# Performance work log

Measured on AMD Instinct MI355X. Metric: run time of the kernel, lower is better.

## Reference

```python
import jax, jax.numpy as jnp
import numpy as np

B, T, E = 4, 2048, 768
H = 12
D = E // H  # head dim = 64


def setup_inputs() -> dict:
    key = jax.random.key(0)
    ks = jax.random.split(key, 9)
    s = 0.02
    x = jax.random.normal(ks[0], (B, T, E), dtype=jnp.float32)
    Wq = jax.random.normal(ks[1], (E, E), dtype=jnp.float32) * s
    bq = jnp.zeros((E,), dtype=jnp.float32)
    Wk = jax.random.normal(ks[2], (E, E), dtype=jnp.float32) * s
    bk = jnp.zeros((E,), dtype=jnp.float32)
    Wv = jax.random.normal(ks[3], (E, E), dtype=jnp.float32) * s
    bv = jnp.zeros((E,), dtype=jnp.float32)
    Wo = jax.random.normal(ks[4], (E, E), dtype=jnp.float32) * s
    bo = jnp.zeros((E,), dtype=jnp.float32)
    # causal mask, broadcastable [1,1,T,T]; masked_fill where mask == 0
    attn_mask = jnp.tril(jnp.ones((T, T), dtype=jnp.int32))[None, None, :, :]
    return {"x": x, "Wq": Wq, "bq": bq, "Wk": Wk, "bk": bk,
            "Wv": Wv, "bv": bv, "Wo": Wo, "bo": bo, "attn_mask": attn_mask}


def reference(x, Wq, bq, Wk, bk, Wv, bv, Wo, bo, attn_mask):
    # QKV projections: [B,T,E] -> [B,T,E]
    q = x @ Wq + bq
    k = x @ Wk + bk
    v = x @ Wv + bv
    # split heads -> [B,H,T,D]
    def split(t):
        return t.reshape(B, T, H, D).transpose(0, 2, 1, 3)
    q, k, v = split(q), split(k), split(v)
    # eager attention: full [B,H,T,T] scores (faithful to the torch module)
    att = jnp.einsum('bhqd,bhkd->bhqk', q, k) * (1.0 / np.sqrt(D).astype(np.float32))
    att = jnp.where(attn_mask == 0, jnp.float32(-jnp.inf), att)
    att_weights = jax.nn.softmax(att, axis=-1)
    # attn_dropout rate = 0.0 (eval) -> identity
    y = jnp.einsum('bhqk,bhkd->bhqd', att_weights, v)
    y = y.transpose(0, 2, 1, 3).reshape(B, T, E)
    y = y @ Wo + bo  # proj_dropout rate = 0.0 -> identity
    return (y, att_weights)
```

## Files before the change

### kernel.cpp

```cpp
#include <hip/hip_runtime.h>
#include <hip/hip_bf16.h>
#include <stdint.h>

#define BB 4
#define HH 12
#define TT 2048
#define DD 64
#define EE 768
#define BT (BB*TT)
#define NQKV (3*EE)

typedef __attribute__((ext_vector_type(8))) short bf16x8;
typedef __attribute__((ext_vector_type(4))) float f32x4;

__device__ __forceinline__ unsigned short f2bf(float f){
  union { float f; unsigned int u; } x; x.f = f;
  unsigned int u = x.u;
  unsigned int r = (u + 0x7fffu + ((u >> 16) & 1u)) >> 16;
  return (unsigned short)r;
}

__global__ void cvt_bf16(const float* __restrict__ src, unsigned short* __restrict__ dst, int n){
  int i = (blockIdx.x*blockDim.x + threadIdx.x)*4;
  if (i < n){
    float4 v = *(const float4*)&src[i];
    ushort4 o;
    o.x = f2bf(v.x); o.y = f2bf(v.y); o.z = f2bf(v.z); o.w = f2bf(v.w);
    *(ushort4*)&dst[i] = o;
  }
}

__global__ void transpose_cvt_768(const float* __restrict__ src,
                                  unsigned short* __restrict__ dst){
  __shared__ float tile[32][33];
  int bx = blockIdx.x*32, by = blockIdx.y*32;
  int tx = threadIdx.x, ty = threadIdx.y;
  #pragma unroll
  for (int i=0;i<32;i+=8) tile[ty+i][tx] = src[(size_t)(by+ty+i)*EE + bx+tx];
  __syncthreads();
  #pragma unroll
  for (int i=0;i<32;i+=8) dst[(size_t)(bx+ty+i)*EE + by+tx] = f2bf(tile[tx][ty+i]);
}

__device__ __forceinline__ void gemm_core_128(
    const unsigned short* __restrict__ A, const unsigned short* __restrict__ Bt,
    int K, int mBase, int nBase,
    unsigned short* Alds, unsigned short* Blds,
    f32x4 acc[4][4])
{
  const int tid = threadIdx.x;
  const int lane = tid & 63, wave = tid >> 6;
  const int wm = wave & 1, wn = wave >> 1;
  const int ln15 = lane & 15, quad = lane >> 4;
  #pragma unroll
  for (int mt=0; mt<4; ++mt)
    #pragma unroll
    for (int nt=0; nt<4; ++nt)
      acc[mt][nt] = (f32x4){0.f,0.f,0.f,0.f};

  for (int k0=0; k0<K; k0+=32){
    #pragma unroll
    for (int i=0;i<2;i++){
      int idx = tid + i*256;
      int r = idx >> 2, seg = idx & 3;
      *(uint4*)&Alds[r*40 + seg*8] = *(const uint4*)&A[(size_t)(mBase + r)*K + k0 + seg*8];
      *(uint4*)&Blds[r*40 + seg*8] = *(const uint4*)&Bt[(size_t)(nBase + r)*K + k0 + seg*8];
    }
    __syncthreads();
    bf16x8 af[4], bfr[4];
    #pragma unroll
    for (int mt=0;mt<4;++mt) af[mt]  = *(const bf16x8*)&Alds[(wm*64 + mt*16 + ln15)*40 + quad*8];
    #pragma unroll
    for (int nt=0;nt<4;++nt) bfr[nt] = *(const bf16x8*)&Blds[(wn*64 + nt*16 + ln15)*40 + quad*8];
    #pragma unroll
    for (int mt=0;mt<4;++mt)
      #pragma unroll
      for (int nt=0;nt<4;++nt)
        acc[mt][nt] = __builtin_amdgcn_mfma_f32_16x16x32_bf16(af[mt], bfr[nt], acc[mt][nt], 0,0,0);
    __syncthreads();
  }
}

#define QSCALE 0.18033688f
__global__ __launch_bounds__(256,2) void gemm_qkv(
    const unsigned short* __restrict__ x, const unsigned short* __restrict__ WtQKV,
    const float* __restrict__ bq, const float* __restrict__ bk,
    const float* __restrict__ bv,
    unsigned short* __restrict__ q_ws, unsigned short* __restrict__ k_ws,
    unsigned short* __restrict__ v_ws)
{
  __shared__ unsigned short Alds[128*40];
  __shared__ unsigned short Blds[128*40];
  const int mBase = blockIdx.y*128, nBase = blockIdx.x*128;
  f32x4 acc[4][4];
  gemm_core_128(x, WtQKV, EE, mBase, nBase, Alds, Blds, acc);

  const int tid = threadIdx.x, lane = tid&63, wave = tid>>6;
  const int wm = wave&1, wn = wave>>1, ln15 = lane&15, quad = lane>>4;
  const int which = nBase / EE;
  const float* bias = (which==0) ? bq : ((which==1) ? bk : bv);
  const float sc = (which==0) ? QSCALE : 1.0f;
  #pragma unroll
  for (int nt=0;nt<4;++nt){
    int col = nBase + wn*64 + nt*16 + ln15;
    int n0 = col - which*EE;
    int h = n0 >> 6, d = n0 & 63;
    float bsv = bias[n0];
    #pragma unroll
    for (int mt=0;mt<4;++mt){
      #pragma unroll
      for (int reg=0;reg<4;++reg){
        int row = mBase + wm*64 + mt*16 + quad*4 + reg;
        int b = row >> 11, t = row & 2047;
        unsigned short o = f2bf((acc[mt][nt][reg] + bsv)*sc);
        if (which==0)      q_ws[((size_t)(b*HH + h)*TT + t)*DD + d] = o;
        else if (which==1) k_ws[((size_t)(b*HH + h)*TT + t)*DD + d] = o;
        else               v_ws[((size_t)(b*HH + h)*DD + d)*TT + t] = o;
      }
    }
  }
}

__global__ __launch_bounds__(256,2) void gemm_proj(
    const unsigned short* __restrict__ yin, const unsigned short* __restrict__ WoT,
    const float* __restrict__ bo, float* __restrict__ out)
{
  __shared__ unsigned short Alds[128*40];
  __shared__ unsigned short Blds[128*40];
  const int mBase = blockIdx.y*128, nBase = blockIdx.x*128;
  f32x4 acc[4][4];
  gemm_core_128(yin, WoT, EE, mBase, nBase, Alds, Blds, acc);

  const int tid = threadIdx.x, lane = tid&63, wave = tid>>6;
  const int wm = wave&1, wn = wave>>1, ln15 = lane&15, quad = lane>>4;
  #pragma unroll
  for (int nt=0;nt<4;++nt){
    int col = nBase + wn*64 + nt*16 + ln15;
    float bsv = bo[col];
    #pragma unroll
    for (int mt=0;mt<4;++mt){
      #pragma unroll
      for (int reg=0;reg<4;++reg){
        int row = mBase + wm*64 + mt*16 + quad*4 + reg;
        out[(size_t)row*EE + col] = acc[mt][nt][reg] + bsv;
      }
    }
  }
}

__global__ __launch_bounds__(256,2) void attn_kernel(
    const unsigned short* __restrict__ q_ws, const unsigned short* __restrict__ k_ws,
    const unsigned short* __restrict__ v_ws, float* __restrict__ att,
    unsigned short* __restrict__ y_ws)
{
  const int sid = blockIdx.x;
  const int qt  = (sid >> 3) & 31;
  const int bh  = (sid & 7) + ((sid >> 8) << 3);
  const int b  = bh / HH, h = bh - b*HH;
  const int tid = threadIdx.x, lane = tid&63, wave = tid>>6;
  const int quad = lane>>4, ln15 = lane&15;

  __shared__ unsigned short Qs[64*72];
  __shared__ unsigned short Ks[2][64*72];
  __shared__ unsigned short Vts[2][64*72];
  __shared__ unsigned short Ps[4*16*72];

  const unsigned short* Qg = q_ws + ((size_t)bh*TT + qt*64)*DD;
  const unsigned short* Kg = k_ws + (size_t)bh*TT*DD;
  const unsigned short* Vg = v_ws + (size_t)bh*DD*TT;
  float* attb = att + ((size_t)bh*TT + (size_t)qt*64)*TT;

  const int r0 = tid>>3, sg = tid&7;
  const int r1 = r0 + 32;

  uint4 ka0 = *(const uint4*)&Kg[(size_t)r0*DD + sg*8];
  uint4 ka1 = *(const uint4*)&Kg[(size_t)r1*DD + sg*8];

  *(uint4*)&Qs[r0*72 + sg*8] = *(const uint4*)&Qg[(size_t)r0*DD + sg*8];
  *(uint4*)&Qs[r1*72 + sg*8] = *(const uint4*)&Qg[(size_t)r1*DD + sg*8];
  __syncthreads();
  bf16x8 aq0 = *(const bf16x8*)&Qs[(wave*16+ln15)*72 + quad*8];
  bf16x8 aq1 = *(const bf16x8*)&Qs[(wave*16+ln15)*72 + 32 + quad*8];

  const float NEG = -30000.0f;
  const int qrow0 = qt*64 + wave*16 + quad*4;

  float lp[4] = {0.f,0.f,0.f,0.f};
  for (int kt=0; kt<=qt; ++kt){
    unsigned short* Kb = Ks[kt&1];
    *(uint4*)&Kb[r0*72 + sg*8] = ka0;
    *(uint4*)&Kb[r1*72 + sg*8] = ka1;
    __syncthreads();
    if (kt < qt){
      ka0 = *(const uint4*)&Kg[(size_t)((kt+1)*64+r0)*DD + sg*8];
      ka1 = *(const uint4*)&Kg[(size_t)((kt+1)*64+r1)*DD + sg*8];
    }
    f32x4 s[4];
    #pragma unroll
    for (int nt=0;nt<4;++nt){
      s[nt] = (f32x4){0.f,0.f,0.f,0.f};
      bf16x8 bk0 = *(const bf16x8*)&Kb[(nt*16+ln15)*72 + quad*8];
      bf16x8 bk1 = *(const bf16x8*)&Kb[(nt*16+ln15)*72 + 32 + quad*8];
      s[nt] = __builtin_amdgcn_mfma_f32_16x16x32_bf16(aq0, bk0, s[nt], 0,0,0);
      s[nt] = __builtin_amdgcn_mfma_f32_16x16x32_bf16(aq1, bk1, s[nt], 0,0,0);
    }
    const bool diag = (kt==qt);
    #pragma unroll
    for (int reg=0;reg<4;++reg){
      #pragma unroll
      for (int nt=0;nt<4;++nt){
        float v = s[nt][reg];
        if (diag && (kt*64 + nt*16 + ln15) > qrow0+reg) v = NEG;
        lp[reg] += exp2f(v);
      }
    }
  }
  float rl[4];
  #pragma unroll
  for (int r=0;r<4;++r){
    float ss = lp[r];
    ss += __shfl_xor(ss, 1);
    ss += __shfl_xor(ss, 2);
    ss += __shfl_xor(ss, 4);
    ss += __shfl_xor(ss, 8);
    rl[r] = 1.f / ss;
  }

  f32x4 yacc[4];
  #pragma unroll
  for (int nt=0;nt<4;++nt) yacc[nt] = (f32x4){0.f,0.f,0.f,0.f};

  uint4 kb0 = *(const uint4*)&Kg[(size_t)r0*DD + sg*8];
  uint4 kb1 = *(const uint4*)&Kg[(size_t)r1*DD + sg*8];
  uint4 vb0 = *(const uint4*)&Vg[(size_t)r0*TT + sg*8];
  uint4 vb1 = *(const uint4*)&Vg[(size_t)r1*TT + sg*8];
  __syncthreads();

  for (int kt=0; kt<=qt; ++kt){
    unsigned short* Kb = Ks[kt&1];
    unsigned short* Vb = Vts[kt&1];
    *(uint4*)&Kb[r0*72 + sg*8] = kb0;
    *(uint4*)&Kb[r1*72 + sg*8] = kb1;
    *(uint4*)&Vb[r0*72 + sg*8] = vb0;
    *(uint4*)&Vb[r1*72 + sg*8] = vb1;
    __syncthreads();
    if (kt < qt){
      kb0 = *(const uint4*)&Kg[(size_t)((kt+1)*64+r0)*DD + sg*8];
      kb1 = *(const uint4*)&Kg[(size_t)((kt+1)*64+r1)*DD + sg*8];
      vb0 = *(const uint4*)&Vg[(size_t)r0*TT + (kt+1)*64 + sg*8];
      vb1 = *(const uint4*)&Vg[(size_t)r1*TT + (kt+1)*64 + sg*8];
    }
    f32x4 s[4];
    #pragma unroll
    for (int nt=0;nt<4;++nt){
      s[nt] = (f32x4){0.f,0.f,0.f,0.f};
      bf16x8 bk0 = *(const bf16x8*)&Kb[(nt*16+ln15)*72 + quad*8];
      bf16x8 bk1 = *(const bf16x8*)&Kb[(nt*16+ln15)*72 + 32 + quad*8];
      s[nt] = __builtin_amdgcn_mfma_f32_16x16x32_bf16(aq0, bk0, s[nt], 0,0,0);
      s[nt] = __builtin_amdgcn_mfma_f32_16x16x32_bf16(aq1, bk1, s[nt], 0,0,0);
    }
    const bool diag = (kt==qt);
    #pragma unroll
    for (int nt=0;nt<4;++nt){
      int key = kt*64 + nt*16 + ln15;
      #pragma unroll
      for (int reg=0;reg<4;++reg){
        float v = s[nt][reg];
        if (diag && key > qrow0+reg) v = NEG;
        float p = exp2f(v)*rl[reg];
        attb[(size_t)(wave*16 + quad*4 + reg)*TT + key] = p;
        Ps[wave*1152 + (quad*4+reg)*72 + nt*16 + ln15] = f2bf(p);
      }
    }
    bf16x8 ap0 = *(const bf16x8*)&Ps[(wave*16+ln15)*72 + quad*8];
    bf16x8 ap1 = *(const bf16x8*)&Ps[(wave*16+ln15)*72 + 32 + quad*8];
    #pragma unroll
    for (int nt=0;nt<4;++nt){
      bf16x8 bv0 = *(const bf16x8*)&Vb[(nt*16+ln15)*72 + quad*8];
      bf16x8 bv1 = *(const bf16x8*)&Vb[(nt*16+ln15)*72 + 32 + quad*8];
      yacc[nt] = __builtin_amdgcn_mfma_f32_16x16x32_bf16(ap0, bv0, yacc[nt], 0,0,0);
      yacc[nt] = __builtin_amdgcn_mfma_f32_16x16x32_bf16(ap1, bv1, yacc[nt], 0,0,0);
    }
  }

  {
    int wstart = (qt+1)*64;
    int r = tid>>2;
    float4 z = make_float4(0.f,0.f,0.f,0.f);
    for (int c = wstart + (tid&3)*4; c < TT; c += 16)
      *(float4*)&attb[(size_t)r*TT + c] = z;
  }

  #pragma unroll
  for (int nt=0;nt<4;++nt){
    #pragma unroll
    for (int reg=0;reg<4;++reg){
      int t = qt*64 + wave*16 + quad*4 + reg;
      size_t row = (size_t)b*TT + t;
      int col = h*DD + nt*16 + ln15;
      y_ws[row*EE + col] = f2bf(yacc[nt][reg]);
    }
  }
}

extern "C" void kernel_launch(void* const* d_in, const int* in_sizes, int n_in,
                              void* d_out, int out_size, void* d_ws, size_t ws_size,
                              hipStream_t stream){
  (void)in_sizes; (void)n_in; (void)out_size; (void)ws_size;
  const float* x  = (const float*)d_in[0];
  const float* Wq = (const float*)d_in[1];
  const float* bq = (const float*)d_in[2];
  const float* Wk = (const float*)d_in[3];
  const float* bk = (const float*)d_in[4];
  const float* Wv = (const float*)d_in[5];
  const float* bv = (const float*)d_in[6];
  const float* Wo = (const float*)d_in[7];
  const float* bo = (const float*)d_in[8];

  float* out = (float*)d_out;
  float* y_out   = out;
  float* att_out = out + (size_t)BT*EE;

  unsigned short* ws = (unsigned short*)d_ws;
  unsigned short* x_bf   = ws;
  unsigned short* WtQKV  = x_bf  + (size_t)BT*EE;
  unsigned short* WoT    = WtQKV + (size_t)NQKV*EE;
  unsigned short* q_ws   = WoT   + (size_t)EE*EE;
  unsigned short* k_ws   = q_ws  + (size_t)BB*HH*TT*DD;
  unsigned short* v_ws   = k_ws  + (size_t)BB*HH*TT*DD;
  unsigned short* y_ws   = v_ws  + (size_t)BB*HH*TT*DD;

  cvt_bf16<<<(BT*EE)/(256*4), 256, 0, stream>>>(x, x_bf, BT*EE);
  dim3 tb(32,8), tg(24,24);
  transpose_cvt_768<<<tg, tb, 0, stream>>>(Wq, WtQKV);
  transpose_cvt_768<<<tg, tb, 0, stream>>>(Wk, WtQKV + (size_t)EE*EE);
  transpose_cvt_768<<<tg, tb, 0, stream>>>(Wv, WtQKV + (size_t)2*EE*EE);
  transpose_cvt_768<<<tg, tb, 0, stream>>>(Wo, WoT);

  gemm_qkv<<<dim3(NQKV/128, BT/128), 256, 0, stream>>>(x_bf, WtQKV, bq, bk, bv, q_ws, k_ws, v_ws);
  attn_kernel<<<dim3(32*BB*HH), 256, 0, stream>>>(q_ws, k_ws, v_ws, att_out, y_ws);
  gemm_proj<<<dim3(EE/128, BT/128), 256, 0, stream>>>(y_ws, WoT, bo, y_out);
}
```

Before: 1.115 ms.

## Process two query tiles per attention block to share K/V tile loads

Each attention workgroup now handles 128 query rows (two 64-row subtiles) instead of 64, so each K and V tile staged into shared memory is reused by both subtiles, roughly halving K/V global traffic and LDS staging. The grid is halved and query tiles are scheduled in descending order so the longest causal blocks start first. The cost is more registers for the doubled accumulators and Q fragments, which may reduce occupancy, and fewer, larger blocks that can leave CUs idle at the tail.

```diff
diff --git a/kernel.cpp b/kernel.cpp
--- a/kernel.cpp
+++ b/kernel.cpp
@@ -153,152 +153,186 @@
     const unsigned short* __restrict__ v_ws, float* __restrict__ att,
     unsigned short* __restrict__ y_ws)
 {
-  const int sid = blockIdx.x;
-  const int qt  = (sid >> 3) & 31;
-  const int bh  = (sid & 7) + ((sid >> 8) << 3);
-  const int b  = bh / HH, h = bh - b*HH;
-  const int tid = threadIdx.x, lane = tid&63, wave = tid>>6;
-  const int quad = lane>>4, ln15 = lane&15;
-
-  __shared__ unsigned short Qs[64*72];
+  const int bid  = blockIdx.x;
+  const int grp  = bid >> 7;
+  const int qt   = 15 - ((bid >> 3) & 15);
+  const int bh   = (bid & 7) | (grp << 3);
+  const int b    = bh / HH;
+  const int h    = bh - b*HH;
+  const int tid  = threadIdx.x;
+  const int lane = tid & 63, wave = tid >> 6;
+  const int quad = lane >> 4, ln15 = lane & 15;
+  const int q0   = 2*qt;
+  const int q1   = q0 + 1;
+  const int qbase = qt*128;
+
+  __shared__ unsigned short Qs[128*72];
   __shared__ unsigned short Ks[2][64*72];
   __shared__ unsigned short Vts[2][64*72];
   __shared__ unsigned short Ps[4*16*72];
 
-  const unsigned short* Qg = q_ws + ((size_t)bh*TT + qt*64)*DD;
+  const unsigned short* Qg = q_ws + ((size_t)bh*TT + qbase)*DD;
   const unsigned short* Kg = k_ws + (size_t)bh*TT*DD;
   const unsigned short* Vg = v_ws + (size_t)bh*DD*TT;
-  float* attb = att + ((size_t)bh*TT + (size_t)qt*64)*TT;
-
-  const int r0 = tid>>3, sg = tid&7;
-  const int r1 = r0 + 32;
-
-  uint4 ka0 = *(const uint4*)&Kg[(size_t)r0*DD + sg*8];
-  uint4 ka1 = *(const uint4*)&Kg[(size_t)r1*DD + sg*8];
-
-  *(uint4*)&Qs[r0*72 + sg*8] = *(const uint4*)&Qg[(size_t)r0*DD + sg*8];
-  *(uint4*)&Qs[r1*72 + sg*8] = *(const uint4*)&Qg[(size_t)r1*DD + sg*8];
+  float* attb = att + ((size_t)bh*TT + (size_t)qbase)*TT;
+
+  const int seg  = tid & 7;
+  const int rowA = tid >> 3;
+  const int rowB = rowA + 32;
+
+  uint4 pkA = *(const uint4*)&Kg[(size_t)rowA*DD + seg*8];
+  uint4 pkB = *(const uint4*)&Kg[(size_t)rowB*DD + seg*8];
+
+  #pragma unroll
+  for (int i=0;i<4;i++){
+    int r = rowA + i*32;
+    *(uint4*)&Qs[r*72 + seg*8] = *(const uint4*)&Qg[(size_t)r*DD + seg*8];
+  }
   __syncthreads();
-  bf16x8 aq0 = *(const bf16x8*)&Qs[(wave*16+ln15)*72 + quad*8];
-  bf16x8 aq1 = *(const bf16x8*)&Qs[(wave*16+ln15)*72 + 32 + quad*8];
+  bf16x8 aq[2][2];
+  #pragma unroll
+  for (int st=0; st<2; ++st){
+    aq[st][0] = *(const bf16x8*)&Qs[(st*64 + wave*16+ln15)*72 + quad*8];
+    aq[st][1] = *(const bf16x8*)&Qs[(st*64 + wave*16+ln15)*72 + 32 + quad*8];
+  }
 
   const float NEG = -30000.0f;
-  const int qrow0 = qt*64 + wave*16 + quad*4;
-
-  float lp[4] = {0.f,0.f,0.f,0.f};
-  for (int kt=0; kt<=qt; ++kt){
+
+  float lp[2][4] = {{0.f,0.f,0.f,0.f},{0.f,0.f,0.f,0.f}};
+  for (int kt=0; kt<=q1; ++kt){
     unsigned short* Kb = Ks[kt&1];
-    *(uint4*)&Kb[r0*72 + sg*8] = ka0;
-    *(uint4*)&Kb[r1*72 + sg*8] = ka1;
+    *(uint4*)&Kb[rowA*72 + seg*8] = pkA;
+    *(uint4*)&Kb[rowB*72 + seg*8] = pkB;
     __syncthreads();
-    if (kt < qt){
-      ka0 = *(const uint4*)&Kg[(size_t)((kt+1)*64+r0)*DD + sg*8];
-      ka1 = *(const uint4*)&Kg[(size_t)((kt+1)*64+r1)*DD + sg*8];
-    }
-    f32x4 s[4];
-    #pragma unroll
-    for (int nt=0;nt<4;++nt){
-      s[nt] = (f32x4){0.f,0.f,0.f,0.f};
-      bf16x8 bk0 = *(const bf16x8*)&Kb[(nt*16+ln15)*72 + quad*8];
-      bf16x8 bk1 = *(const bf16x8*)&Kb[(nt*16+ln15)*72 + 32 + quad*8];
-      s[nt] = __builtin_amdgcn_mfma_f32_16x16x32_bf16(aq0, bk0, s[nt], 0,0,0);
-      s[nt] = __builtin_amdgcn_mfma_f32_16x16x32_bf16(aq1, bk1, s[nt], 0,0,0);
-    }
-    const bool diag = (kt==qt);
-    #pragma unroll
-    for (int reg=0;reg<4;++reg){
-      #pragma unroll
-      for (int nt=0;nt<4;++nt){
-        float v = s[nt][reg];
-        if (diag && (kt*64 + nt*16 + ln15) > qrow0+reg) v = NEG;
-        lp[reg] += exp2f(v);
-      }
-    }
-  }
-  float rl[4];
-  #pragma unroll
-  for (int r=0;r<4;++r){
-    float ss = lp[r];
-    ss += __shfl_xor(ss, 1);
-    ss += __shfl_xor(ss, 2);
-    ss += __shfl_xor(ss, 4);
-    ss += __shfl_xor(ss, 8);
-    rl[r] = 1.f / ss;
-  }
-
-  f32x4 yacc[4];
-  #pragma unroll
-  for (int nt=0;nt<4;++nt) yacc[nt] = (f32x4){0.f,0.f,0.f,0.f};
-
-  uint4 kb0 = *(const uint4*)&Kg[(size_t)r0*DD + sg*8];
-  uint4 kb1 = *(const uint4*)&Kg[(size_t)r1*DD + sg*8];
-  uint4 vb0 = *(const uint4*)&Vg[(size_t)r0*TT + sg*8];
-  uint4 vb1 = *(const uint4*)&Vg[(size_t)r1*TT + sg*8];
+    if (kt < q1){
+      pkA = *(const uint4*)&Kg[(size_t)((kt+1)*64+rowA)*DD + seg*8];
+      pkB = *(const uint4*)&Kg[(size_t)((kt+1)*64+rowB)*DD + seg*8];
+    }
+    #pragma unroll
+    for (int st=0; st<2; ++st){
+      if (kt <= q0 + st){
+        f32x4 s[4];
+        #pragma unroll
+        for (int nt=0;nt<4;++nt){
+          s[nt] = (f32x4){0.f,0.f,0.f,0.f};
+          bf16x8 bk0 = *(const bf16x8*)&Kb[(nt*16+ln15)*72 + quad*8];
+          bf16x8 bk1 = *(const bf16x8*)&Kb[(nt*16+ln15)*72 + 32 + quad*8];
+          s[nt] = __builtin_amdgcn_mfma_f32_16x16x32_bf16(aq[st][0], bk0, s[nt], 0,0,0);
+          s[nt] = __builtin_amdgcn_mfma_f32_16x16x32_bf16(aq[st][1], bk1, s[nt], 0,0,0);
+        }
+        const bool diag = (kt == q0 + st);
+        const int qr0 = qbase + st*64 + wave*16 + quad*4;
+        #pragma unroll
+        for (int reg=0;reg<4;++reg){
+          #pragma unroll
+          for (int nt=0;nt<4;++nt){
+            float v = s[nt][reg];
+            if (diag && (kt*64 + nt*16 + ln15) > qr0+reg) v = NEG;
+            lp[st][reg] += exp2f(v);
+          }
+        }
+      }
+    }
+  }
+  float rl[2][4];
+  #pragma unroll
+  for (int st=0; st<2; ++st){
+    #pragma unroll
+    for (int r=0;r<4;++r){
+      float ss = lp[st][r];
+      ss += __shfl_xor(ss, 1);
+      ss += __shfl_xor(ss, 2);
+      ss += __shfl_xor(ss, 4);
+      ss += __shfl_xor(ss, 8);
+      rl[st][r] = 1.f / ss;
+    }
+  }
+
+  f32x4 yacc[2][4];
+  #pragma unroll
+  for (int st=0; st<2; ++st)
+    #pragma unroll
+    for (int nt=0;nt<4;++nt) yacc[st][nt] = (f32x4){0.f,0.f,0.f,0.f};
+
+  uint4 pk2A = *(const uint4*)&Kg[(size_t)rowA*DD + seg*8];
+  uint4 pk2B = *(const uint4*)&Kg[(size_t)rowB*DD + seg*8];
+  uint4 pvA  = *(const uint4*)&Vg[(size_t)rowA*TT + seg*8];
+  uint4 pvB  = *(const uint4*)&Vg[(size_t)rowB*TT + seg*8];
   __syncthreads();
 
-  for (int kt=0; kt<=qt; ++kt){
+  for (int kt=0; kt<=q1; ++kt){
     unsigned short* Kb = Ks[kt&1];
     unsigned short* Vb = Vts[kt&1];
-    *(uint4*)&Kb[r0*72 + sg*8] = kb0;
-    *(uint4*)&Kb[r1*72 + sg*8] = kb1;
-    *(uint4*)&Vb[r0*72 + sg*8] = vb0;
-    *(uint4*)&Vb[r1*72 + sg*8] = vb1;
+    *(uint4*)&Kb[rowA*72 + seg*8] = pk2A;
+    *(uint4*)&Kb[rowB*72 + seg*8] = pk2B;
+    *(uint4*)&Vb[rowA*72 + seg*8] = pvA;
+    *(uint4*)&Vb[rowB*72 + seg*8] = pvB;
     __syncthreads();
-    if (kt < qt){
-      kb0 = *(const uint4*)&Kg[(size_t)((kt+1)*64+r0)*DD + sg*8];
-      kb1 = *(const uint4*)&Kg[(size_t)((kt+1)*64+r1)*DD + sg*8];
-      vb0 = *(const uint4*)&Vg[(size_t)r0*TT + (kt+1)*64 + sg*8];
-      vb1 = *(const uint4*)&Vg[(size_t)r1*TT + (kt+1)*64 + sg*8];
-    }
-    f32x4 s[4];
+    if (kt < q1){
+      pk2A = *(const uint4*)&Kg[(size_t)((kt+1)*64+rowA)*DD + seg*8];
+      pk2B = *(const uint4*)&Kg[(size_t)((kt+1)*64+rowB)*DD + seg*8];
+      pvA  = *(const uint4*)&Vg[(size_t)rowA*TT + (kt+1)*64 + seg*8];
+      pvB  = *(const uint4*)&Vg[(size_t)rowB*TT + (kt+1)*64 + seg*8];
+    }
+    #pragma unroll
+    for (int st=0; st<2; ++st){
+      if (kt <= q0 + st){
+        f32x4 s[4];
+        #pragma unroll
+        for (int nt=0;nt<4;++nt){
+          s[nt] = (f32x4){0.f,0.f,0.f,0.f};
+          bf16x8 bk0 = *(const bf16x8*)&Kb[(nt*16+ln15)*72 + quad*8];
+          bf16x8 bk1 = *(const bf16x8*)&Kb[(nt*16+ln15)*72 + 32 + quad*8];
+          s[nt] = __builtin_amdgcn_mfma_f32_16x16x32_bf16(aq[st][0], bk0, s[nt], 0,0,0);
+          s[nt] = __builtin_amdgcn_mfma_f32_16x16x32_bf16(aq[st][1], bk1, s[nt], 0,0,0);
+        }
+        const bool diag = (kt == q0 + st);
+        const int qr0 = qbase + st*64 + wave*16 + quad*4;
+        #pragma unroll
+        for (int nt=0;nt<4;++nt){
+          int key = kt*64 + nt*16 + ln15;
+          #pragma unroll
+          for (int reg=0;reg<4;++reg){
+            float v = s[nt][reg];
+            if (diag && key > qr0+reg) v = NEG;
+            float p = exp2f(v)*rl[st][reg];
+            attb[(size_t)(st*64 + wave*16 + quad*4 + reg)*TT + key] = p;
+            Ps[wave*1152 + (quad*4+reg)*72 + nt*16 + ln15] = f2bf(p);
+          }
+        }
+        bf16x8 ap0 = *(const bf16x8*)&Ps[(wave*16+ln15)*72 + quad*8];
+        bf16x8 ap1 = *(const bf16x8*)&Ps[(wave*16+ln15)*72 + 32 + quad*8];
+        #pragma unroll
+        for (int nt=0;nt<4;++nt){
+          bf16x8 bv0 = *(const bf16x8*)&Vb[(nt*16+ln15)*72 + quad*8];
+          bf16x8 bv1 = *(const bf16x8*)&Vb[(nt*16+ln15)*72 + 32 + quad*8];
+          yacc[st][nt] = __builtin_amdgcn_mfma_f32_16x16x32_bf16(ap0, bv0, yacc[st][nt], 0,0,0);
+          yacc[st][nt] = __builtin_amdgcn_mfma_f32_16x16x32_bf16(ap1, bv1, yacc[st][nt], 0,0,0);
+        }
+      }
+    }
+  }
+
+  #pragma unroll
+  for (int half=0; half<2; ++half){
+    int r = (tid>>2) + half*64;
+    int cstart = (q0 + half + 1)*64 + (tid&3)*4;
+    float4 z = make_float4(0.f,0.f,0.f,0.f);
+    for (int c = cstart; c < TT; c += 16)
+      *(float4*)&attb[(size_t)r*TT + c] = z;
+  }
+
+  #pragma unroll
+  for (int st=0; st<2; ++st){
     #pragma unroll
     for (int nt=0;nt<4;++nt){
-      s[nt] = (f32x4){0.f,0.f,0.f,0.f};
-      bf16x8 bk0 = *(const bf16x8*)&Kb[(nt*16+ln15)*72 + quad*8];
-      bf16x8 bk1 = *(const bf16x8*)&Kb[(nt*16+ln15)*72 + 32 + quad*8];
-      s[nt] = __builtin_amdgcn_mfma_f32_16x16x32_bf16(aq0, bk0, s[nt], 0,0,0);
-      s[nt] = __builtin_amdgcn_mfma_f32_16x16x32_bf16(aq1, bk1, s[nt], 0,0,0);
-    }
-    const bool diag = (kt==qt);
-    #pragma unroll
-    for (int nt=0;nt<4;++nt){
-      int key = kt*64 + nt*16 + ln15;
       #pragma unroll
       for (int reg=0;reg<4;++reg){
-        float v = s[nt][reg];
-        if (diag && key > qrow0+reg) v = NEG;
-        float p = exp2f(v)*rl[reg];
-        attb[(size_t)(wave*16 + quad*4 + reg)*TT + key] = p;
-        Ps[wave*1152 + (quad*4+reg)*72 + nt*16 + ln15] = f2bf(p);
-      }
-    }
-    bf16x8 ap0 = *(const bf16x8*)&Ps[(wave*16+ln15)*72 + quad*8];
-    bf16x8 ap1 = *(const bf16x8*)&Ps[(wave*16+ln15)*72 + 32 + quad*8];
-    #pragma unroll
-    for (int nt=0;nt<4;++nt){
-      bf16x8 bv0 = *(const bf16x8*)&Vb[(nt*16+ln15)*72 + quad*8];
-      bf16x8 bv1 = *(const bf16x8*)&Vb[(nt*16+ln15)*72 + 32 + quad*8];
-      yacc[nt] = __builtin_amdgcn_mfma_f32_16x16x32_bf16(ap0, bv0, yacc[nt], 0,0,0);
-      yacc[nt] = __builtin_amdgcn_mfma_f32_16x16x32_bf16(ap1, bv1, yacc[nt], 0,0,0);
-    }
-  }
-
-  {
-    int wstart = (qt+1)*64;
-    int r = tid>>2;
-    float4 z = make_float4(0.f,0.f,0.f,0.f);
-    for (int c = wstart + (tid&3)*4; c < TT; c += 16)
-      *(float4*)&attb[(size_t)r*TT + c] = z;
-  }
-
-  #pragma unroll
-  for (int nt=0;nt<4;++nt){
-    #pragma unroll
-    for (int reg=0;reg<4;++reg){
-      int t = qt*64 + wave*16 + quad*4 + reg;
-      size_t row = (size_t)b*TT + t;
-      int col = h*DD + nt*16 + ln15;
-      y_ws[row*EE + col] = f2bf(yacc[nt][reg]);
+        int t = qbase + st*64 + wave*16 + quad*4 + reg;
+        size_t row = (size_t)b*TT + t;
+        int col = h*DD + nt*16 + ln15;
+        y_ws[row*EE + col] = f2bf(yacc[st][nt][reg]);
+      }
     }
   }
 }
@@ -338,6 +372,6 @@
   transpose_cvt_768<<<tg, tb, 0, stream>>>(Wo, WoT);
 
   gemm_qkv<<<dim3(NQKV/128, BT/128), 256, 0, stream>>>(x_bf, WtQKV, bq, bk, bv, q_ws, k_ws, v_ws);
-  attn_kernel<<<dim3(32*BB*HH), 256, 0, stream>>>(q_ws, k_ws, v_ws, att_out, y_ws);
+  attn_kernel<<<dim3(16*BB*HH), 256, 0, stream>>>(q_ws, k_ws, v_ws, att_out, y_ws);
   gemm_proj<<<dim3(EE/128, BT/128), 256, 0, stream>>>(y_ws, WoT, bo, y_out);
 }
```

Result: slower. 1.150 ms (+3.1%).
